# Kernel tuning notes

Measured on AMD Instinct MI355X. Metric: run time of the kernel, lower is better.

## Reference

```python
import jax, jax.numpy as jnp
import numpy as np

N = 100000
IN_DIM = 512
OUT_DIM = 512


def setup_inputs() -> dict:
    key = jax.random.key(0)
    k1, k2, k3, k4 = jax.random.split(key, 4)
    x = jax.random.normal(k1, (N, IN_DIM), dtype=jnp.float32)
    edge_index = jax.random.randint(k2, (2, N), 0, N, dtype=jnp.int64)
    # Linear params (torch nn.Linear: out = x @ W.T + b)
    bound = 1.0 / np.sqrt(IN_DIM)
    W = jax.random.uniform(k3, (OUT_DIM, IN_DIM), minval=-bound, maxval=bound, dtype=jnp.float32)
    b = jax.random.uniform(k4, (OUT_DIM,), minval=-bound, maxval=bound, dtype=jnp.float32)
    return {"x": x, "edge_index": edge_index, "W": W, "b": b}


def reference(x, edge_index, W, b):
    # out = relu(linear(x))
    out = jax.nn.relu(jnp.einsum('ni,oi->no', x, W) + b)  # [N, OUT_DIM]
    # torch.scatter_add(out, 0, col[:, None], x):
    # index has shape [E, 1] so only column 0 of src (= x) is scattered:
    # out[col[e], 0] += x[e, 0]
    col = edge_index[1].astype(jnp.int32)  # [E], E == N here
    E = col.shape[0]
    out = out.at[col, 0].add(x[:E, 0])
    return out
```

## Files before the change

### kernel.cpp

```cpp
#include <hip/hip_runtime.h>
#include <stdint.h>

#define K_DIM 512
#define N_OUT 512
#define BM 128
#define BN 128
#define BK 64

typedef __bf16 bf16x8 __attribute__((ext_vector_type(8)));
typedef float f32x4 __attribute__((ext_vector_type(4)));
typedef unsigned short ushort8 __attribute__((ext_vector_type(8)));

__device__ inline unsigned short f2bf(float f) {
  unsigned u = __float_as_uint(f);
  u += 0x7fffu + ((u >> 16) & 1u);
  return (unsigned short)(u >> 16);
}

__global__ __launch_bounds__(256) void prep_all_kernel(
    const float* __restrict__ x, unsigned short* __restrict__ xb,
    const float* __restrict__ W, unsigned short* __restrict__ wb,
    float* __restrict__ x0, float* __restrict__ s,
    int n8x, int n8w, int n8s) {
  const int stride = gridDim.x * 256;
  const int total = n8x + n8w + n8s;
  for (int i = blockIdx.x * 256 + threadIdx.x; i < total; i += stride) {
    if (i < n8x) {
      const f32x4* sp = (const f32x4*)x + (size_t)i * 2;
      f32x4 a = __builtin_nontemporal_load(sp);
      f32x4 c = __builtin_nontemporal_load(sp + 1);
      ushort8 o;
      o[0] = f2bf(a[0]); o[1] = f2bf(a[1]); o[2] = f2bf(a[2]); o[3] = f2bf(a[3]);
      o[4] = f2bf(c[0]); o[5] = f2bf(c[1]); o[6] = f2bf(c[2]); o[7] = f2bf(c[3]);
      *(ushort8*)(xb + (size_t)i * 8) = o;
      if ((i & 63) == 0) x0[i >> 6] = a[0];
    } else if (i < n8x + n8w) {
      int j = i - n8x;
      const f32x4* sp = (const f32x4*)W + (size_t)j * 2;
      f32x4 a = sp[0], c = sp[1];
      ushort8 o;
      o[0] = f2bf(a[0]); o[1] = f2bf(a[1]); o[2] = f2bf(a[2]); o[3] = f2bf(a[3]);
      o[4] = f2bf(c[0]); o[5] = f2bf(c[1]); o[6] = f2bf(c[2]); o[7] = f2bf(c[3]);
      *(ushort8*)(wb + (size_t)j * 8) = o;
    } else {
      int j = i - n8x - n8w;
      f32x4 z = {0.f, 0.f, 0.f, 0.f};
      *(f32x4*)(s + (size_t)j * 8) = z;
      *(f32x4*)(s + (size_t)j * 8 + 4) = z;
    }
  }
}

__global__ __launch_bounds__(256) void scatter_s_kernel(const float* __restrict__ x0,
                                                        const int* __restrict__ ei,
                                                        float* __restrict__ s, int E) {
  int e = blockIdx.x * 256 + threadIdx.x;
  if (e < E) {
    atomicAdd(s + ei[E + e], x0[e]);
  }
}

__global__ __launch_bounds__(256) void gemm_bf16_kernel(
    const unsigned short* __restrict__ xb, const unsigned short* __restrict__ wb,
    const float* __restrict__ b, const float* __restrict__ s,
    float* __restrict__ out, int M) {
  __shared__ __align__(16) unsigned short Als[BM * BK];
  __shared__ __align__(16) unsigned short Bls[BN * BK];

  const int tid = threadIdx.x;
  const int lane = tid & 63;
  const int quad = lane >> 4;
  const int l16 = lane & 15;
  const int waveId = tid >> 6;
  const int wm = (waveId >> 1) * 64;
  const int wn = (waveId & 1) * 64;

  const int nwg = gridDim.x * gridDim.y;
  int raw = blockIdx.y * gridDim.x + blockIdx.x;
  int q = nwg >> 3, r = nwg & 7;
  int xcd = raw & 7;
  int wg = (xcd < r ? xcd * (q + 1) : r * (q + 1) + (xcd - r) * q) + (raw >> 3);
  const int blockM = (wg >> 2) * BM;
  const int blockN = (wg & 3) * BN;

  size_t goffA[4], goffB[4];
  int ldsoff[4];
#pragma unroll
  for (int i = 0; i < 4; ++i) {
    int ch = i * 256 + tid;
    int row = ch >> 3;
    int c8 = ch & 7;
    int sc = c8 ^ (row & 7);
    int ga_row = blockM + row;
    if (ga_row > M - 1) ga_row = M - 1;
    goffA[i] = (size_t)ga_row * K_DIM + sc * 8;
    goffB[i] = (size_t)(blockN + row) * K_DIM + sc * 8;
    ldsoff[i] = ch * 8;
  }

  f32x4 acc[4][4] = {};

  for (int k0 = 0; k0 < K_DIM; k0 += BK) {
#pragma unroll
    for (int i = 0; i < 4; ++i) {
      __builtin_amdgcn_global_load_lds(
          (const __attribute__((address_space(1))) void*)(xb + goffA[i] + k0),
          (__attribute__((address_space(3))) void*)(&Als[ldsoff[i]]), 16, 0, 0);
      __builtin_amdgcn_global_load_lds(
          (const __attribute__((address_space(1))) void*)(wb + goffB[i] + k0),
          (__attribute__((address_space(3))) void*)(&Bls[ldsoff[i]]), 16, 0, 0);
    }
    __syncthreads();

#pragma unroll
    for (int ss = 0; ss < 2; ++ss) {
      bf16x8 af[4], bfr[4];
#pragma unroll
      for (int mi = 0; mi < 4; ++mi) {
        int rr = wm + mi * 16 + l16;
        int c = (ss * 4 + quad) ^ (rr & 7);
        af[mi] = *(const bf16x8*)(&Als[rr * BK + c * 8]);
      }
#pragma unroll
      for (int ni = 0; ni < 4; ++ni) {
        int rr = wn + ni * 16 + l16;
        int c = (ss * 4 + quad) ^ (rr & 7);
        bfr[ni] = *(const bf16x8*)(&Bls[rr * BK + c * 8]);
      }
#pragma unroll
      for (int mi = 0; mi < 4; ++mi)
#pragma unroll
        for (int ni = 0; ni < 4; ++ni)
          acc[mi][ni] = __builtin_amdgcn_mfma_f32_16x16x32_bf16(af[mi], bfr[ni], acc[mi][ni], 0, 0, 0);
    }
    __syncthreads();
  }

#pragma unroll
  for (int ni = 0; ni < 4; ++ni) {
    int gcol = blockN + wn + ni * 16 + l16;
    float bias = b[gcol];
#pragma unroll
    for (int mi = 0; mi < 4; ++mi) {
#pragma unroll
      for (int rr = 0; rr < 4; ++rr) {
        int grow = blockM + wm + mi * 16 + quad * 4 + rr;
        if (grow < M) {
          float v = acc[mi][ni][rr] + bias;
          v = v > 0.f ? v : 0.f;
          if (gcol == 0) v += s[grow];
          __builtin_nontemporal_store(v, out + (size_t)grow * N_OUT + gcol);
        }
      }
    }
  }
}

#define LDS_STRIDE 40
__global__ __launch_bounds__(256) void gemm_fused_kernel(
    const float* __restrict__ x, const float* __restrict__ W,
    const float* __restrict__ b, float* __restrict__ out, int M) {
  __shared__ __align__(16) unsigned short Als[BM * LDS_STRIDE];
  __shared__ __align__(16) unsigned short Bls[BN * LDS_STRIDE];
  const int tid = threadIdx.x;
  const int lane = tid & 63;
  const int quad = lane >> 4;
  const int l16 = lane & 15;
  const int waveId = tid >> 6;
  const int wm = (waveId >> 1) * 64;
  const int wn = (waveId & 1) * 64;
  const int blockM = blockIdx.y * BM;
  const int blockN = blockIdx.x * BN;
  f32x4 acc[4][4] = {};
  for (int k0 = 0; k0 < K_DIM; k0 += 32) {
#pragma unroll
    for (int i = 0; i < 4; ++i) {
      int idx = i * 256 + tid;
      int row = idx >> 3;
      int c4 = idx & 7;
      float4 va = make_float4(0.f, 0.f, 0.f, 0.f);
      int grow = blockM + row;
      if (grow < M) va = *(const float4*)(x + (size_t)grow * K_DIM + k0 + c4 * 4);
      ushort4 ha;
      ha.x = f2bf(va.x); ha.y = f2bf(va.y); ha.z = f2bf(va.z); ha.w = f2bf(va.w);
      *(ushort4*)(&Als[row * LDS_STRIDE + c4 * 4]) = ha;
      float4 vb = *(const float4*)(W + (size_t)(blockN + row) * K_DIM + k0 + c4 * 4);
      ushort4 hb;
      hb.x = f2bf(vb.x); hb.y = f2bf(vb.y); hb.z = f2bf(vb.z); hb.w = f2bf(vb.w);
      *(ushort4*)(&Bls[row * LDS_STRIDE + c4 * 4]) = hb;
    }
    __syncthreads();
    bf16x8 af[4], bfr[4];
#pragma unroll
    for (int mi = 0; mi < 4; ++mi)
      af[mi] = *(const bf16x8*)(&Als[(wm + mi * 16 + l16) * LDS_STRIDE + quad * 8]);
#pragma unroll
    for (int ni = 0; ni < 4; ++ni)
      bfr[ni] = *(const bf16x8*)(&Bls[(wn + ni * 16 + l16) * LDS_STRIDE + quad * 8]);
#pragma unroll
    for (int mi = 0; mi < 4; ++mi)
#pragma unroll
      for (int ni = 0; ni < 4; ++ni)
        acc[mi][ni] = __builtin_amdgcn_mfma_f32_16x16x32_bf16(af[mi], bfr[ni], acc[mi][ni], 0, 0, 0);
    __syncthreads();
  }
#pragma unroll
  for (int ni = 0; ni < 4; ++ni) {
    int gcol = blockN + wn + ni * 16 + l16;
    float bias = b[gcol];
#pragma unroll
    for (int mi = 0; mi < 4; ++mi) {
#pragma unroll
      for (int rr = 0; rr < 4; ++rr) {
        int grow = blockM + wm + mi * 16 + quad * 4 + rr;
        if (grow < M) {
          float v = acc[mi][ni][rr] + bias;
          out[(size_t)grow * N_OUT + gcol] = v > 0.f ? v : 0.f;
        }
      }
    }
  }
}

__global__ void scatter_kernel(const float* __restrict__ x,
                               const int* __restrict__ ei,
                               float* __restrict__ out, int E) {
  int e = blockIdx.x * 256 + threadIdx.x;
  if (e < E) {
    int c = ei[E + e];
    atomicAdd(out + (size_t)c * N_OUT, x[(size_t)e * K_DIM]);
  }
}

extern "C" void kernel_launch(void* const* d_in, const int* in_sizes, int n_in,
                              void* d_out, int out_size, void* d_ws, size_t ws_size,
                              hipStream_t stream) {
  const float* x = (const float*)d_in[0];
  const int* ei = (const int*)d_in[1];
  const float* W = (const float*)d_in[2];
  const float* b = (const float*)d_in[3];
  float* out = (float*)d_out;

  int M = in_sizes[0] / K_DIM;
  int E = in_sizes[1] / 2;

  size_t x_elems = (size_t)M * K_DIM;
  size_t w_elems = (size_t)N_OUT * K_DIM;
  int n8x = (int)(x_elems / 8);
  int n8w = (int)(w_elems / 8);
  int n8s = (M + 7) / 8;
  size_t s_elems = (size_t)n8s * 8;

  size_t need = x_elems * 2 + w_elems * 2 + s_elems * 4 + (size_t)M * 4;

  dim3 grid(N_OUT / BN, (M + BM - 1) / BM);

  if (ws_size >= need) {
    unsigned short* xb = (unsigned short*)d_ws;
    unsigned short* wb = xb + x_elems;
    float* s = (float*)(wb + w_elems);
    float* x0 = s + s_elems;

    int total = n8x + n8w + n8s;
    int pblk = (total + 255) / 256;
    if (pblk > 2048) pblk = 2048;
    prep_all_kernel<<<pblk, 256, 0, stream>>>(x, xb, W, wb, x0, s, n8x, n8w, n8s);
    scatter_s_kernel<<<(E + 255) / 256, 256, 0, stream>>>(x0, ei, s, E);
    gemm_bf16_kernel<<<grid, 256, 0, stream>>>(xb, wb, b, s, out, M);
  } else {
    gemm_fused_kernel<<<grid, 256, 0, stream>>>(x, W, b, out, M);
    scatter_kernel<<<(E + 255) / 256, 256, 0, stream>>>(x, ei, out, E);
  }
}
```

Baseline: 452.9 us.

## Double-buffer LDS tiles in GEMM to overlap global loads with MFMA

Converts the single-buffered K loop into a two-stage ping-pong pipeline. The next two K tiles are prefetched into alternating LDS buffers, and explicit vmcnt waits allow one tile's loads to stay in flight while MFMAs run on the other. It also raises wave priority around the MFMA block with s_setprio. LDS use doubles to 64KB per block, which may reduce occupancy, and the hand-coded vmcnt counts depend on how many loads each stage issues.

New measurement: 440.2 us. 1.03x faster.

```diff
diff --git a/kernel.cpp b/kernel.cpp
--- a/kernel.cpp
+++ b/kernel.cpp
@@ -6,6 +6,7 @@
 #define BM 128
 #define BN 128
 #define BK 64
+#define NT 8
 
 typedef __bf16 bf16x8 __attribute__((ext_vector_type(8)));
 typedef float f32x4 __attribute__((ext_vector_type(4)));
@@ -64,8 +65,8 @@
     const unsigned short* __restrict__ xb, const unsigned short* __restrict__ wb,
     const float* __restrict__ b, const float* __restrict__ s,
     float* __restrict__ out, int M) {
-  __shared__ __align__(16) unsigned short Als[BM * BK];
-  __shared__ __align__(16) unsigned short Bls[BN * BK];
+  __shared__ __align__(16) unsigned short Als[2][BM * BK];
+  __shared__ __align__(16) unsigned short Bls[2][BN * BK];
 
   const int tid = threadIdx.x;
   const int lane = tid & 63;
@@ -98,20 +99,33 @@
     ldsoff[i] = ch * 8;
   }
 
+#define STAGE(buf, k0)                                                              \
+  {                                                                                 \
+    _Pragma("unroll") for (int i = 0; i < 4; ++i) {                                 \
+      __builtin_amdgcn_global_load_lds(                                             \
+          (const __attribute__((address_space(1))) void*)(xb + goffA[i] + (k0)),    \
+          (__attribute__((address_space(3))) void*)(&Als[buf][ldsoff[i]]), 16, 0, 0);\
+      __builtin_amdgcn_global_load_lds(                                             \
+          (const __attribute__((address_space(1))) void*)(wb + goffB[i] + (k0)),    \
+          (__attribute__((address_space(3))) void*)(&Bls[buf][ldsoff[i]]), 16, 0, 0);\
+    }                                                                               \
+  }
+
   f32x4 acc[4][4] = {};
 
-  for (int k0 = 0; k0 < K_DIM; k0 += BK) {
-#pragma unroll
-    for (int i = 0; i < 4; ++i) {
-      __builtin_amdgcn_global_load_lds(
-          (const __attribute__((address_space(1))) void*)(xb + goffA[i] + k0),
-          (__attribute__((address_space(3))) void*)(&Als[ldsoff[i]]), 16, 0, 0);
-      __builtin_amdgcn_global_load_lds(
-          (const __attribute__((address_space(1))) void*)(wb + goffB[i] + k0),
-          (__attribute__((address_space(3))) void*)(&Bls[ldsoff[i]]), 16, 0, 0);
-    }
-    __syncthreads();
-
+  STAGE(0, 0);
+  STAGE(1, BK);
+
+#pragma unroll
+  for (int t = 0; t < NT; ++t) {
+    if (t < NT - 1) {
+      asm volatile("s_waitcnt vmcnt(8)" ::: "memory");
+    } else {
+      asm volatile("s_waitcnt vmcnt(0)" ::: "memory");
+    }
+    __builtin_amdgcn_s_barrier();
+
+    const int cur = t & 1;
 #pragma unroll
     for (int ss = 0; ss < 2; ++ss) {
       bf16x8 af[4], bfr[4];
@@ -119,22 +133,29 @@
       for (int mi = 0; mi < 4; ++mi) {
         int rr = wm + mi * 16 + l16;
         int c = (ss * 4 + quad) ^ (rr & 7);
-        af[mi] = *(const bf16x8*)(&Als[rr * BK + c * 8]);
+        af[mi] = *(const bf16x8*)(&Als[cur][rr * BK + c * 8]);
       }
 #pragma unroll
       for (int ni = 0; ni < 4; ++ni) {
         int rr = wn + ni * 16 + l16;
         int c = (ss * 4 + quad) ^ (rr & 7);
-        bfr[ni] = *(const bf16x8*)(&Bls[rr * BK + c * 8]);
-      }
+        bfr[ni] = *(const bf16x8*)(&Bls[cur][rr * BK + c * 8]);
+      }
+      __builtin_amdgcn_s_setprio(1);
 #pragma unroll
       for (int mi = 0; mi < 4; ++mi)
 #pragma unroll
         for (int ni = 0; ni < 4; ++ni)
           acc[mi][ni] = __builtin_amdgcn_mfma_f32_16x16x32_bf16(af[mi], bfr[ni], acc[mi][ni], 0, 0, 0);
-    }
-    __syncthreads();
-  }
+      __builtin_amdgcn_s_setprio(0);
+    }
+
+    __builtin_amdgcn_s_barrier();
+    if (t + 2 < NT) {
+      STAGE(cur, (t + 2) * BK);
+    }
+  }
+#undef STAGE
 
 #pragma unroll
   for (int ni = 0; ni < 4; ++ni) {
```
